# Kernel tuning notes

Hardware: AMD Instinct MI355X
Metric: run time of the kernel (lower is better)

## Reference

```python
import jax, jax.numpy as jnp
import numpy as np

EMBED = 1024
HEADS = 16
HEAD_DIM = EMBED // HEADS
MASKED_BIAS = -10000.0


def setup_inputs() -> dict:
    key = jax.random.key(0)
    k1, k2, k3 = jax.random.split(key, 3)
    hidden_states = jax.random.normal(k1, (4, 2048, EMBED), dtype=jnp.float32)
    c_attn_w = jax.random.normal(k2, (EMBED, 3 * EMBED), dtype=jnp.float32) * 0.02
    c_attn_b = jnp.zeros((3 * EMBED,), dtype=jnp.float32)
    c_proj_w = jax.random.normal(k3, (EMBED, EMBED), dtype=jnp.float32) * 0.02
    c_proj_b = jnp.zeros((EMBED,), dtype=jnp.float32)
    return {
        "hidden_states": hidden_states,
        "c_attn_w": c_attn_w,
        "c_attn_b": c_attn_b,
        "c_proj_w": c_proj_w,
        "c_proj_b": c_proj_b,
    }


def reference(hidden_states, c_attn_w, c_attn_b, c_proj_w, c_proj_b):
    B, S, E = hidden_states.shape
    # QKV projection (Conv1D == x @ W + b)
    qkv = hidden_states @ c_attn_w + c_attn_b  # [B,S,3E]
    q, k, v = jnp.split(qkv, 3, axis=-1)
    def split_heads(t):
        return t.reshape(B, S, HEADS, HEAD_DIM).transpose(0, 2, 1, 3)  # [B,H,S,D]
    q, k, v = split_heads(q), split_heads(k), split_heads(v)
    # scaled attention scores
    scores = jnp.einsum("bhqd,bhkd->bhqk", q, k) / jnp.float32(HEAD_DIM) ** 0.5
    causal = jnp.tril(jnp.ones((S, S), dtype=bool))
    scores = jnp.where(causal[None, None], scores, jnp.float32(MASKED_BIAS))
    attn_weights = jax.nn.softmax(scores, axis=-1)
    attn_out = jnp.einsum("bhqk,bhkd->bhqd", attn_weights, v)
    attn_out = attn_out.transpose(0, 2, 1, 3).reshape(B, S, E)
    out = attn_out @ c_proj_w + c_proj_b
    return out
```

## Files before the change

### kernel.cpp

```cpp
#include <hip/hip_runtime.h>
#include <hip/hip_bf16.h>

#define EMB 1024
#define SEQ 2048
#define ATT_SCALE 0.18033688011112042f

typedef __bf16 bf16x8 __attribute__((ext_vector_type(8)));
typedef float f32x4 __attribute__((ext_vector_type(4)));
typedef float f32x16 __attribute__((ext_vector_type(16)));

__device__ __forceinline__ unsigned short f2bf(float f) {
    union { float f; unsigned int u; } v; v.f = f;
    unsigned int r = (v.u + 0x7FFFu + ((v.u >> 16) & 1u)) >> 16;
    return (unsigned short)r;
}

__device__ __forceinline__ void async_load16(const void* g, void* l) {
    __builtin_amdgcn_global_load_lds(
        (const __attribute__((address_space(1))) unsigned int*)g,
        (__attribute__((address_space(3))) unsigned int*)l, 16, 0, 0);
}

__global__ void cvt_bf16(const float4* __restrict__ in, ushort4* __restrict__ out, int n4) {
    int i = blockIdx.x * blockDim.x + threadIdx.x;
    int stride = gridDim.x * blockDim.x;
    for (; i < n4; i += stride) {
        float4 v = in[i];
        ushort4 o;
        o.x = f2bf(v.x); o.y = f2bf(v.y); o.z = f2bf(v.z); o.w = f2bf(v.w);
        out[i] = o;
    }
}

__global__ void transpose_cvt(const float* __restrict__ in, unsigned short* __restrict__ out,
                              int R, int C) {
    __shared__ float tile[32][33];
    int bx = blockIdx.x * 32;
    int by = blockIdx.y * 32;
    int tx = threadIdx.x & 31;
    int ty = threadIdx.x >> 5;
    #pragma unroll
    for (int i = 0; i < 32; i += 8)
        tile[ty + i][tx] = in[(size_t)(by + ty + i) * C + bx + tx];
    __syncthreads();
    #pragma unroll
    for (int i = 0; i < 32; i += 8)
        out[(size_t)(bx + ty + i) * R + by + tx] = f2bf(tile[tx][ty + i]);
}

#define BM 128
#define BN 128
#define BK 64

template<bool OUT_BF16>
__global__ __launch_bounds__(256, 2)
void gemm_bf16(const unsigned short* __restrict__ A,
               const unsigned short* __restrict__ Bt,
               const float* __restrict__ bias,
               void* __restrict__ Cout,
               int M, int N, int K) {
    __shared__ unsigned short As[BM * 64];
    __shared__ unsigned short Bs[BN * 64];
    const int tid = threadIdx.x;
    const int m0 = blockIdx.y * BM;
    const int n0 = blockIdx.x * BN;
    const int lane = tid & 63;
    const int wave = tid >> 6;
    const int wm = (wave & 1) * 64;
    const int wn = (wave >> 1) * 64;
    const int lm = lane & 15;
    const int quad = lane >> 4;
    const int r8 = lane >> 3;
    const int pc = lane & 7;

    f32x4 acc[4][4] = {};

    for (int k0 = 0; k0 < K; k0 += BK) {
        __syncthreads();
        #pragma unroll
        for (int i = 0; i < 4; i++) {
            int r = wave * 32 + i * 8 + r8;
            int lc = pc ^ (r & 7);
            async_load16(&A[(size_t)(m0 + r) * K + k0 + lc * 8], &As[(wave * 32 + i * 8) * 64]);
            async_load16(&Bt[(size_t)(n0 + r) * K + k0 + lc * 8], &Bs[(wave * 32 + i * 8) * 64]);
        }
        __syncthreads();
        #pragma unroll
        for (int kk = 0; kk < 2; kk++) {
            bf16x8 af[4], bfr[4];
            #pragma unroll
            for (int t = 0; t < 4; t++) {
                int phys = ((kk * 4 + quad) ^ (lm & 7)) << 3;
                af[t]  = *(const bf16x8*)&As[(wm + t * 16 + lm) * 64 + phys];
                bfr[t] = *(const bf16x8*)&Bs[(wn + t * 16 + lm) * 64 + phys];
            }
            #pragma unroll
            for (int mt = 0; mt < 4; mt++)
                #pragma unroll
                for (int nt = 0; nt < 4; nt++)
                    acc[mt][nt] = __builtin_amdgcn_mfma_f32_16x16x32_bf16(
                        af[mt], bfr[nt], acc[mt][nt], 0, 0, 0);
        }
    }
    #pragma unroll
    for (int mt = 0; mt < 4; mt++) {
        #pragma unroll
        for (int nt = 0; nt < 4; nt++) {
            int col = n0 + wn + nt * 16 + lm;
            float bv = bias[col];
            #pragma unroll
            for (int r = 0; r < 4; r++) {
                int row = m0 + wm + mt * 16 + quad * 4 + r;
                float val = acc[mt][nt][r] + bv;
                if (OUT_BF16)
                    ((unsigned short*)Cout)[(size_t)row * N + col] = f2bf(val);
                else
                    ((float*)Cout)[(size_t)row * N + col] = val;
            }
        }
    }
}

__global__ void transpose_v(const unsigned short* __restrict__ qkv,
                            unsigned short* __restrict__ vt) {
    __shared__ unsigned short T[64 * 72];
    const int tid = threadIdx.x;
    const int sb = blockIdx.x;
    const int bh = blockIdx.y;
    const int b = bh >> 4;
    const int h = bh & 15;
    const unsigned short* src = qkv + (size_t)(b * SEQ + sb * 64) * 3072 + 2 * EMB + h * 64;
    #pragma unroll
    for (int i = 0; i < 2; i++) {
        int c = tid + 256 * i;
        int row = c >> 3;
        int col = (c & 7) * 8;
        *(uint4*)&T[row * 72 + col] = *(const uint4*)&src[(size_t)row * 3072 + col];
    }
    __syncthreads();
    unsigned short* dst = vt + (size_t)bh * 64 * SEQ + sb * 64;
    #pragma unroll
    for (int i = 0; i < 2; i++) {
        int c = tid + 256 * i;
        int dr = c >> 3;
        int sc = (c & 7) * 8;
        unsigned short tmp[8];
        #pragma unroll
        for (int j = 0; j < 8; j++) tmp[j] = T[(sc + j) * 72 + dr];
        *(uint4*)&dst[(size_t)dr * SEQ + sc] = *(uint4*)tmp;
    }
}

__global__ __launch_bounds__(256, 4)
void attention(const unsigned short* __restrict__ qkv,
               const unsigned short* __restrict__ vt,
               unsigned short* __restrict__ outb) {
    __shared__ unsigned short smem[4 * 64 * 72];
    const int tid = threadIdx.x;
    const int lane = tid & 63;
    const int wave = tid >> 6;
    const int l31 = lane & 31;
    const int half = lane >> 5;
    const int bh = blockIdx.x;
    const int b = bh >> 4;
    const int h = bh & 15;
    const int srow0 = tid >> 3;
    const int sch  = (tid & 7) * 8;

    const int qt = 15 - (int)blockIdx.y;
    const int qs = qt * 128 + wave * 32 + l31;
    const size_t qgrow = (size_t)b * SEQ + qs;

    bf16x8 qf[4];
    #pragma unroll
    for (int dt = 0; dt < 4; dt++)
        qf[dt] = *(const bf16x8*)&qkv[qgrow * 3072 + h * 64 + dt * 16 + half * 8];

    f32x16 o[2] = {};
    float m_prev = -1e30f, lsum = 0.f;

    const int nkb = 2 * qt + 2;
    const int qmax_w = qt * 128 + wave * 32 + 31;

    uint4 kreg[2], vreg[2];
    #pragma unroll
    for (int i = 0; i < 2; i++) {
        int row = srow0 + 32 * i;
        kreg[i] = *(const uint4*)&qkv[(size_t)(b * SEQ + row) * 3072 + EMB + h * 64 + sch];
        vreg[i] = *(const uint4*)&vt[(size_t)(bh * 64 + row) * SEQ + sch];
    }

    for (int kb = 0; kb < nkb; kb++) {
        unsigned short* Ks = smem + (kb & 1) * 2 * 64 * 72;
        unsigned short* Vs = Ks + 64 * 72;
        #pragma unroll
        for (int i = 0; i < 2; i++) {
            int row = srow0 + 32 * i;
            *(uint4*)&Ks[row * 72 + sch] = kreg[i];
            *(uint4*)&Vs[row * 72 + sch] = vreg[i];
        }
        if (kb + 1 < nkb) {
            #pragma unroll
            for (int i = 0; i < 2; i++) {
                int row = srow0 + 32 * i;
                kreg[i] = *(const uint4*)&qkv[(size_t)(b * SEQ + (kb + 1) * 64 + row) * 3072 + EMB + h * 64 + sch];
                vreg[i] = *(const uint4*)&vt[(size_t)(bh * 64 + row) * SEQ + (kb + 1) * 64 + sch];
            }
        }
        __syncthreads();

        if (kb * 64 > qmax_w) continue;

        f32x16 st[2] = {};
        #pragma unroll
        for (int dt = 0; dt < 4; dt++) {
            #pragma unroll
            for (int ct = 0; ct < 2; ct++) {
                bf16x8 kf = *(const bf16x8*)&Ks[(ct * 32 + l31) * 72 + dt * 16 + half * 8];
                st[ct] = __builtin_amdgcn_mfma_f32_32x32x16_bf16(kf, qf[dt], st[ct], 0, 0, 0);
            }
        }

        if (kb * 64 + 63 > qt * 128 + wave * 32) {
            #pragma unroll
            for (int ct = 0; ct < 2; ct++)
                #pragma unroll
                for (int r = 0; r < 16; r++) {
                    int cg = kb * 64 + ct * 32 + (r & 3) + 8 * (r >> 2) + 4 * half;
                    if (cg > qs) st[ct][r] = -1e9f;
                }
        }

        float tm[8];
        #pragma unroll
        for (int r = 0; r < 8; r++)
            tm[r] = fmaxf(fmaxf(st[0][r], st[1][r]), fmaxf(st[0][r + 8], st[1][r + 8]));
        #pragma unroll
        for (int s = 4; s > 0; s >>= 1)
            #pragma unroll
            for (int r = 0; r < s; r++) tm[r] = fmaxf(tm[r], tm[r + s]);
        float mx = fmaxf(tm[0], __shfl_xor(tm[0], 32, 64));
        float m_new = fmaxf(m_prev, mx);
        float alpha = exp2f((m_prev - m_new) * ATT_SCALE);
        float nmc = -m_new * ATT_SCALE;
        #pragma unroll
        for (int r = 0; r < 16; r++) {
            st[0][r] = exp2f(__builtin_fmaf(st[0][r], ATT_SCALE, nmc));
            st[1][r] = exp2f(__builtin_fmaf(st[1][r], ATT_SCALE, nmc));
        }
        float ts[8];
        #pragma unroll
        for (int r = 0; r < 8; r++)
            ts[r] = (st[0][r] + st[1][r]) + (st[0][r + 8] + st[1][r + 8]);
        #pragma unroll
        for (int s = 4; s > 0; s >>= 1)
            #pragma unroll
            for (int r = 0; r < s; r++) ts[r] += ts[r + s];
        float sum = ts[0] + __shfl_xor(ts[0], 32, 64);
        lsum = lsum * alpha + sum;
        m_prev = m_new;
        #pragma unroll
        for (int r = 0; r < 16; r++) { o[0][r] *= alpha; o[1][r] *= alpha; }

        unsigned int pk[2][8];
        #pragma unroll
        for (int t = 0; t < 2; t++)
            #pragma unroll
            for (int i = 0; i < 8; i++) {
                __hip_bfloat162 pb = __float22bfloat162_rn(float2{st[t][2 * i], st[t][2 * i + 1]});
                union { __hip_bfloat162 b; unsigned int u; } cv; cv.b = pb;
                pk[t][i] = cv.u;
            }

        #pragma unroll
        for (int kt = 0; kt < 4; kt++) {
            const int t = kt >> 1, e = kt & 1;
            unsigned int own0 = half ? pk[t][4 * e + 2] : pk[t][4 * e + 0];
            unsigned int own1 = half ? pk[t][4 * e + 3] : pk[t][4 * e + 1];
            unsigned int snd0 = half ? pk[t][4 * e + 0] : pk[t][4 * e + 2];
            unsigned int snd1 = half ? pk[t][4 * e + 1] : pk[t][4 * e + 3];
            unsigned int rcv0 = (unsigned int)__shfl_xor((int)snd0, 32, 64);
            unsigned int rcv1 = (unsigned int)__shfl_xor((int)snd1, 32, 64);
            union { uint4 u; bf16x8 v; } pf;
            pf.u.x = half ? rcv0 : own0;
            pf.u.y = half ? rcv1 : own1;
            pf.u.z = half ? own0 : rcv0;
            pf.u.w = half ? own1 : rcv1;
            #pragma unroll
            for (int dt = 0; dt < 2; dt++) {
                bf16x8 vf = *(const bf16x8*)&Vs[(dt * 32 + l31) * 72 + kt * 16 + half * 8];
                o[dt] = __builtin_amdgcn_mfma_f32_32x32x16_bf16(vf, pf.v, o[dt], 0, 0, 0);
            }
        }
    }

    __syncthreads();
    float inv = 1.0f / lsum;
    #pragma unroll
    for (int dt = 0; dt < 2; dt++)
        #pragma unroll
        for (int r = 0; r < 16; r++) {
            int d = dt * 32 + (r & 3) + 8 * (r >> 2) + 4 * half;
            smem[(wave * 32 + l31) * 72 + d] = f2bf(o[dt][r] * inv);
        }
    __syncthreads();
    #pragma unroll
    for (int i = 0; i < 4; i++) {
        int c = tid + 256 * i;
        int row = c >> 3;
        int ch = (c & 7) * 8;
        uint4 v = *(const uint4*)&smem[row * 72 + ch];
        *(uint4*)&outb[(size_t)(b * SEQ + qt * 128 + row) * EMB + h * 64 + ch] = v;
    }
}

extern "C" void kernel_launch(void* const* d_in, const int* in_sizes, int n_in,
                              void* d_out, int out_size, void* d_ws, size_t ws_size,
                              hipStream_t stream) {
    const float* X     = (const float*)d_in[0];
    const float* Wqkv  = (const float*)d_in[1];
    const float* bqkv  = (const float*)d_in[2];
    const float* Wproj = (const float*)d_in[3];
    const float* bproj = (const float*)d_in[4];
    float* out = (float*)d_out;

    char* ws = (char*)d_ws;
    unsigned short* Xb     = (unsigned short*)(ws);
    unsigned short* WqkvT  = (unsigned short*)(ws + 16777216);
    unsigned short* WprojT = (unsigned short*)(ws + 23068672);
    unsigned short* qkvb   = (unsigned short*)(ws + 25165824);
    unsigned short* Vt     = (unsigned short*)(ws + 75497472);
    unsigned short* attnb  = (unsigned short*)(ws + 92274688);

    cvt_bf16<<<2048, 256, 0, stream>>>((const float4*)X, (ushort4*)Xb, (4 * 2048 * 1024) / 4);
    transpose_cvt<<<dim3(3072 / 32, 1024 / 32), 256, 0, stream>>>(Wqkv, WqkvT, 1024, 3072);
    transpose_cvt<<<dim3(1024 / 32, 1024 / 32), 256, 0, stream>>>(Wproj, WprojT, 1024, 1024);
    gemm_bf16<true><<<dim3(3072 / BN, 8192 / BM), 256, 0, stream>>>(
        Xb, WqkvT, bqkv, qkvb, 8192, 3072, 1024);
    transpose_v<<<dim3(32, 64), 256, 0, stream>>>(qkvb, Vt);
    attention<<<dim3(64, 16), 256, 0, stream>>>(qkvb, Vt, attnb);
    gemm_bf16<false><<<dim3(1024 / BN, 8192 / BM), 256, 0, stream>>>(
        attnb, WprojT, bproj, out, 8192, 1024, 1024);
}
```

Before: 303.8 us.

## Fuse V transpose into QKV GEMM epilogue and remap blocks per XCD

Writes the V third of the QKV projection directly into the transposed Vt layout from the GEMM epilogue, removing the separate transpose_v kernel and its extra read/write pass. Also switches the GEMM to a 1D grid with an XCD-aware mapping that assigns contiguous N-stripes to each XCD, aiming to improve L2 reuse of weight tiles. The fused path writes strided 8-byte stores into Vt and no longer writes V into qkvb, which is fine since attention reads V from Vt.

Result: no change. 301.3 us (-0.8%).

```diff
diff --git a/kernel.cpp b/kernel.cpp
--- a/kernel.cpp
+++ b/kernel.cpp
@@ -52,18 +52,24 @@
 #define BN 128
 #define BK 64
 
-template<bool OUT_BF16>
+template<bool OUT_BF16, bool FUSE_VT>
 __global__ __launch_bounds__(256, 2)
 void gemm_bf16(const unsigned short* __restrict__ A,
                const unsigned short* __restrict__ Bt,
                const float* __restrict__ bias,
                void* __restrict__ Cout,
+               unsigned short* __restrict__ Vtout,
                int M, int N, int K) {
     __shared__ unsigned short As[BM * 64];
     __shared__ unsigned short Bs[BN * 64];
     const int tid = threadIdx.x;
-    const int m0 = blockIdx.y * BM;
-    const int n0 = blockIdx.x * BN;
+    const int id = blockIdx.x;
+    const int nb = N >> 7;
+    const int nper = nb >> 3;
+    const int xcd = id & 7;
+    const int loc = id >> 3;
+    const int m0 = (loc / nper) * BM;
+    const int n0 = (xcd * nper + (loc % nper)) * BN;
     const int lane = tid & 63;
     const int wave = tid >> 6;
     const int wm = (wave & 1) * 64;
@@ -108,46 +114,29 @@
         for (int nt = 0; nt < 4; nt++) {
             int col = n0 + wn + nt * 16 + lm;
             float bv = bias[col];
-            #pragma unroll
-            for (int r = 0; r < 4; r++) {
-                int row = m0 + wm + mt * 16 + quad * 4 + r;
-                float val = acc[mt][nt][r] + bv;
-                if (OUT_BF16)
-                    ((unsigned short*)Cout)[(size_t)row * N + col] = f2bf(val);
-                else
-                    ((float*)Cout)[(size_t)row * N + col] = val;
-            }
-        }
-    }
-}
-
-__global__ void transpose_v(const unsigned short* __restrict__ qkv,
-                            unsigned short* __restrict__ vt) {
-    __shared__ unsigned short T[64 * 72];
-    const int tid = threadIdx.x;
-    const int sb = blockIdx.x;
-    const int bh = blockIdx.y;
-    const int b = bh >> 4;
-    const int h = bh & 15;
-    const unsigned short* src = qkv + (size_t)(b * SEQ + sb * 64) * 3072 + 2 * EMB + h * 64;
-    #pragma unroll
-    for (int i = 0; i < 2; i++) {
-        int c = tid + 256 * i;
-        int row = c >> 3;
-        int col = (c & 7) * 8;
-        *(uint4*)&T[row * 72 + col] = *(const uint4*)&src[(size_t)row * 3072 + col];
-    }
-    __syncthreads();
-    unsigned short* dst = vt + (size_t)bh * 64 * SEQ + sb * 64;
-    #pragma unroll
-    for (int i = 0; i < 2; i++) {
-        int c = tid + 256 * i;
-        int dr = c >> 3;
-        int sc = (c & 7) * 8;
-        unsigned short tmp[8];
-        #pragma unroll
-        for (int j = 0; j < 8; j++) tmp[j] = T[(sc + j) * 72 + dr];
-        *(uint4*)&dst[(size_t)dr * SEQ + sc] = *(uint4*)tmp;
+            if (FUSE_VT && col >= 2 * EMB) {
+                int dd = col - 2 * EMB;
+                int row0 = m0 + wm + mt * 16 + quad * 4;
+                int b = row0 >> 11;
+                int s = row0 & 2047;
+                ushort4 o;
+                o.x = f2bf(acc[mt][nt][0] + bv);
+                o.y = f2bf(acc[mt][nt][1] + bv);
+                o.z = f2bf(acc[mt][nt][2] + bv);
+                o.w = f2bf(acc[mt][nt][3] + bv);
+                *(ushort4*)&Vtout[((size_t)(b * 16) * 64 + dd) * SEQ + s] = o;
+            } else {
+                #pragma unroll
+                for (int r = 0; r < 4; r++) {
+                    int row = m0 + wm + mt * 16 + quad * 4 + r;
+                    float val = acc[mt][nt][r] + bv;
+                    if (OUT_BF16)
+                        ((unsigned short*)Cout)[(size_t)row * N + col] = f2bf(val);
+                    else
+                        ((float*)Cout)[(size_t)row * N + col] = val;
+                }
+            }
+        }
     }
 }
 
@@ -335,10 +324,9 @@
     cvt_bf16<<<2048, 256, 0, stream>>>((const float4*)X, (ushort4*)Xb, (4 * 2048 * 1024) / 4);
     transpose_cvt<<<dim3(3072 / 32, 1024 / 32), 256, 0, stream>>>(Wqkv, WqkvT, 1024, 3072);
     transpose_cvt<<<dim3(1024 / 32, 1024 / 32), 256, 0, stream>>>(Wproj, WprojT, 1024, 1024);
-    gemm_bf16<true><<<dim3(3072 / BN, 8192 / BM), 256, 0, stream>>>(
-        Xb, WqkvT, bqkv, qkvb, 8192, 3072, 1024);
-    transpose_v<<<dim3(32, 64), 256, 0, stream>>>(qkvb, Vt);
+    gemm_bf16<true, true><<<(3072 / BN) * (8192 / BM), 256, 0, stream>>>(
+        Xb, WqkvT, bqkv, qkvb, Vt, 8192, 3072, 1024);
     attention<<<dim3(64, 16), 256, 0, stream>>>(qkvb, Vt, attnb);
-    gemm_bf16<false><<<dim3(1024 / BN, 8192 / BM), 256, 0, stream>>>(
-        attnb, WprojT, bproj, out, 8192, 1024, 1024);
-}
+    gemm_bf16<false, false><<<(1024 / BN) * (8192 / BM), 256, 0, stream>>>(
+        attnb, WprojT, bproj, out, nullptr, 8192, 1024, 1024);
+}
```
